# Kernel optimization log

Measured on AMD Instinct MI355X. Metric: run time of the kernel, lower is better.

## Reference

```python
import jax, jax.numpy as jnp
import numpy as np

B, C, H, W = 4, 256, 64, 64
CI = 3
TEMPERATURE = 0.0001 * 5
EPS = 2.220446049250313e-16  # sys.float_info.epsilon


def _nearest_up4(x):
    # nn.Upsample(scale_factor=4, mode='nearest'): [B,C,H,W] -> [B,C,4H,4W]
    return jnp.repeat(jnp.repeat(x, 4, axis=2), 4, axis=3)


def _avg_pool2(x):
    # AvgPool2d(kernel=2, stride=2, pad=0)
    b, c, h, w = x.shape
    return x.reshape(b, c, h // 2, 2, w // 2, 2).mean(axis=(3, 5))


def _center_norm(feats):
    # subtract per-channel spatial mean, then L2-normalize over channels per position
    b, c, h, w = feats.shape
    t = feats.reshape(b, c, h * w)
    t = t - t.mean(axis=-1, keepdims=True)
    n = jnp.linalg.norm(t, axis=1, keepdims=True) + EPS
    return t / n  # [B,C,HW]


def setup_inputs() -> dict:
    key = jax.random.key(0)
    k1, k2, k3 = jax.random.split(key, 3)
    return {
        "x_feats": jax.random.normal(k1, (B, C, H, W), jnp.float32),
        "y_feats": jax.random.normal(k2, (B, C, H, W), jnp.float32),
        "y_img": jax.random.uniform(k3, (B, CI, 4 * H, 4 * W), jnp.float32),
    }


def reference(x_feats, y_feats, y_img):
    b, c, h, w = x_feats.shape
    hw = h * w
    theta = _center_norm(x_feats)  # [B,C,HW]
    phi = _center_norm(y_feats)    # [B,C,HW]
    f = jnp.einsum('bcm,bcn->bmn', theta, phi)  # dense correlation [B,HW,HW]
    loss_feat_pair = jnp.mean(jnp.abs(theta - phi))  # F.l1_loss(theta, phi)
    # WTA_scale_weight == 1 -> WTA branch bypassed, just temperature scaling
    f_wta = f / TEMPERATURE
    f_div_c = jax.nn.softmax(f_wta, axis=-1)  # [B,HW,HW]
    # warped features: f_div_C @ y_feats^T
    b_lab = y_feats.reshape(b, c, hw)
    y = jnp.einsum('bmn,bcn->bcm', f_div_c, b_lab).reshape(b, c, h, w)
    # soft-argmax coordinates
    xc = (jnp.arange(hw) % w).astype(x_feats.dtype)   # [HW]
    yc = (jnp.arange(hw) // w).astype(x_feats.dtype)  # [HW]
    coords_x = f_div_c @ xc  # [B,HW]
    coords_y = f_div_c @ yc  # [B,HW]
    coords1 = jnp.stack([coords_x, coords_y], axis=1).reshape(b, 2, h, w)
    coords0 = jnp.stack([xc, yc], axis=0).reshape(1, 2, h, w)
    flow = _nearest_up4(coords1 - coords0)  # [B,2,4H,4W]
    # image warping branch (y_img is not None)
    yi = _avg_pool2(_avg_pool2(y_img))  # [B,CI,H,W]
    ci = yi.shape[1]
    yi_flat = yi.reshape(b, ci, hw)
    y_img_attn = jnp.einsum('bmn,bcn->bmc', f_div_c, yi_flat)  # [B,HW,CI]
    f_div_c_v = jax.nn.softmax(jnp.swapaxes(f_wta, 1, 2), axis=-1)
    y_img_cyc = jnp.einsum('bmn,bnc->bcm', f_div_c_v, y_img_attn).reshape(b, ci, h, w)
    y_img_out = jnp.swapaxes(y_img_attn, 1, 2).reshape(b, ci, h, w)
    return (y, flow, _nearest_up4(y_img_out), _nearest_up4(y_img_cyc), loss_feat_pair)
```

## Files before the change

kernel.cpp:

```cpp
#include <hip/hip_runtime.h>
#include <math.h>

#define HW   4096
#define NCH  256
#define NB   4

constexpr float TEMP  = (float)(0.0001 * 5.0);
constexpr float INV_T = 1.0f / TEMP;
constexpr float EPSN  = 2.220446049250313e-16f;

typedef __attribute__((ext_vector_type(8))) _Float16 f16x8;
typedef __attribute__((ext_vector_type(4))) float    f32x4;

constexpr size_t OFF_YT    = 0;
constexpr size_t OFF_YI    = OFF_YT    + (size_t)NB*HW*NCH;
constexpr size_t OFF_MEAN  = OFF_YI    + (size_t)NB*3*HW;
constexpr size_t OFF_RNORM = OFF_MEAN  + (size_t)2*NB*NCH;
constexpr size_t OFF_NSQP  = OFF_RNORM + (size_t)2*NB*HW;
constexpr size_t OFF_F     = OFF_NSQP  + (size_t)2*NB*8*HW;
constexpr size_t OFF_YP    = OFF_F     + (size_t)HW*HW;
constexpr size_t OFF_ROWP  = OFF_YP;
constexpr size_t OFF_COLP  = OFF_YP + (size_t)32*7*HW;
constexpr size_t OFF_RMAX  = OFF_YP    + (size_t)8*NCH*HW;
constexpr size_t OFF_RSUM  = OFF_RMAX  + HW;
constexpr size_t OFF_CMAX  = OFF_RSUM  + HW;
constexpr size_t OFF_CSUM  = OFF_CMAX  + HW;
constexpr size_t OFF_COORD = OFF_CSUM  + HW;
constexpr size_t OFF_ATTN  = OFF_COORD + (size_t)NB*2*HW;
constexpr size_t OFF_CYC   = OFF_ATTN  + (size_t)NB*HW*3;
constexpr size_t OFF_CYCP  = OFF_CYC   + (size_t)NB*3*HW;
constexpr size_t OFF_LOSSP = OFF_CYCP  + (size_t)32*3*HW;
constexpr size_t OFF_F16   = OFF_LOSSP + 1024;

constexpr size_t OUT_Y    = 0;
constexpr size_t OUT_FLOW = (size_t)NB*NCH*HW;
constexpr size_t OUT_IMG  = OUT_FLOW + (size_t)NB*2*256*256;
constexpr size_t OUT_CYCO = OUT_IMG  + (size_t)NB*3*256*256;
constexpr size_t OUT_LOSS = OUT_CYCO + (size_t)NB*3*256*256;

__device__ __forceinline__ void gload16(const void* g, void* l) {
    __builtin_amdgcn_global_load_lds(
        (const __attribute__((address_space(1))) unsigned int*)g,
        (__attribute__((address_space(3))) unsigned int*)l, 16, 0, 0);
}

__global__ void mean_kernel(const float* __restrict__ xf, const float* __restrict__ yf,
                            float* __restrict__ means) {
    const float* src = (blockIdx.y == 0 ? xf : yf) + (size_t)blockIdx.x * HW;
    float s = 0.f;
    for (int i = threadIdx.x; i < HW; i += 256) s += src[i];
    __shared__ float red[256];
    red[threadIdx.x] = s; __syncthreads();
    for (int st = 128; st > 0; st >>= 1) {
        if (threadIdx.x < st) red[threadIdx.x] += red[threadIdx.x + st];
        __syncthreads();
    }
    if (threadIdx.x == 0) means[blockIdx.y * (NB*NCH) + blockIdx.x] = red[0] * (1.0f / HW);
}

__global__ void nsq_partial_kernel(const float* __restrict__ xf, const float* __restrict__ yf,
                                   const float* __restrict__ means, float* __restrict__ part) {
    int t = blockIdx.z >> 2, b = blockIdx.z & 3;
    int m = blockIdx.x * 256 + threadIdx.x;
    int c0 = blockIdx.y * 32;
    const float* src = (t == 0 ? xf : yf) + (size_t)b * NCH * HW;
    const float* mn = means + t * (NB*NCH) + b * NCH;
    float acc = 0.f;
    for (int c = c0; c < c0 + 32; ++c) {
        float v = src[(size_t)c * HW + m] - mn[c];
        acc += v * v;
    }
    part[(((size_t)t*NB + b) * 8 + blockIdx.y) * HW + m] = acc;
}

__global__ void nsq_combine_kernel(const float* __restrict__ part, float* __restrict__ rnorms) {
    int t = blockIdx.y >> 2, b = blockIdx.y & 3;
    int m = blockIdx.x * 256 + threadIdx.x;
    const float* p = part + ((size_t)t*NB + b) * 8 * HW + m;
    float s = 0.f;
    for (int k = 0; k < 8; ++k) s += p[(size_t)k * HW];
    rnorms[((size_t)t*NB + b) * HW + m] = 1.0f / (sqrtf(s) + EPSN);
}

__global__ void ycast_kernel(const float* __restrict__ yf, _Float16* __restrict__ yf16) {
    size_t i = ((size_t)blockIdx.x * 256 + threadIdx.x) * 8;
    const float4* s = (const float4*)(yf + i);
    float4 v0 = s[0], v1 = s[1];
    f16x8 o;
    o[0]=(_Float16)v0.x; o[1]=(_Float16)v0.y; o[2]=(_Float16)v0.z; o[3]=(_Float16)v0.w;
    o[4]=(_Float16)v1.x; o[5]=(_Float16)v1.y; o[6]=(_Float16)v1.z; o[7]=(_Float16)v1.w;
    *(f16x8*)(yf16 + i) = o;
}

__global__ void prep_kernel(const float* __restrict__ xf, const float* __restrict__ yf,
                            const float* __restrict__ means,
                            _Float16* __restrict__ th, _Float16* __restrict__ tl,
                            _Float16* __restrict__ ph, _Float16* __restrict__ pl, int b) {
    __shared__ float tile[32][33];
    int t = blockIdx.z;
    int c0 = blockIdx.x * 32, m0 = blockIdx.y * 32;
    const float* src = (t == 0 ? xf : yf) + (size_t)b * NCH * HW;
    const float* mn  = means + t * (NB*NCH) + b * NCH;
    int tx = threadIdx.x & 31, ty = threadIdx.x >> 5;
    for (int i = ty; i < 32; i += 8)
        tile[i][tx] = src[(size_t)(c0 + i) * HW + m0 + tx] - mn[c0 + i];
    __syncthreads();
    _Float16* H = (t == 0 ? th : ph);
    _Float16* L = (t == 0 ? tl : pl);
    for (int i = ty; i < 32; i += 8) {
        float v = tile[tx][i];
        _Float16 h = (_Float16)v;
        _Float16 l = (_Float16)(v - (float)h);
        H[(size_t)(m0 + i)*NCH + c0 + tx] = h;
        L[(size_t)(m0 + i)*NCH + c0 + tx] = l;
    }
}

__global__ void avgpool_kernel(const float* __restrict__ yimg, float* __restrict__ yi) {
    size_t idx = (size_t)blockIdx.x * 256 + threadIdx.x;
    int m  = (int)(idx & (HW - 1));
    int bc = (int)(idx >> 12);
    int h = m >> 6, w = m & 63;
    const float* p = yimg + (size_t)bc * 65536 + (size_t)(h*4) * 256 + w*4;
    float s = 0.f;
    #pragma unroll
    for (int dy = 0; dy < 4; ++dy) {
        #pragma unroll
        for (int dx = 0; dx < 4; ++dx) s += p[dy*256 + dx];
    }
    yi[idx] = s * (1.0f/16.0f);
}

__global__ __launch_bounds__(256) void gemm_f_kernel(
        const _Float16* __restrict__ th, const _Float16* __restrict__ tl,
        const _Float16* __restrict__ ph, const _Float16* __restrict__ pl,
        const float* __restrict__ rnorms, const float* __restrict__ yi,
        float* __restrict__ f, float* __restrict__ rowp, float* __restrict__ colp,
        int b) {
    __shared__ char lds[2][4][8192];
    int tid  = threadIdx.x;
    int lane = tid & 63;
    int w = tid >> 6, wm = w >> 1, wn = w & 1;
    int m0 = blockIdx.y * 128, n0 = blockIdx.x * 128;

    int o0 = tid * 16, o1 = o0 + 4096;
    int r0 = o0 >> 6, s0 = (o0 >> 4) & 3, g0 = s0 ^ ((r0 >> 1) & 3);
    int r1 = o1 >> 6, s1 = (o1 >> 4) & 3, g1 = s1 ^ ((r1 >> 1) & 3);
    size_t ga0 = (size_t)(n0 + r0)*NCH + g0*8;
    size_t ga1 = (size_t)(n0 + r1)*NCH + g1*8;
    size_t gb0 = (size_t)(m0 + r0)*NCH + g0*8;
    size_t gb1 = (size_t)(m0 + r1)*NCH + g1*8;

    int fra = wm*64 + (lane & 15);
    int frb = wn*64 + (lane & 15);
    int ks  = lane >> 4;

    auto STAGE = [&](int buf, int k0) {
        gload16(ph + ga0 + k0, &lds[buf][0][o0]);
        gload16(ph + ga1 + k0, &lds[buf][0][o1]);
        gload16(pl + ga0 + k0, &lds[buf][1][o0]);
        gload16(pl + ga1 + k0, &lds[buf][1][o1]);
        gload16(th + gb0 + k0, &lds[buf][2][o0]);
        gload16(th + gb1 + k0, &lds[buf][2][o1]);
        gload16(tl + gb0 + k0, &lds[buf][3][o0]);
        gload16(tl + gb1 + k0, &lds[buf][3][o1]);
    };

    f32x4 acc[4][4];
    #pragma unroll
    for (int i = 0; i < 4; ++i)
        #pragma unroll
        for (int j = 0; j < 4; ++j) acc[i][j] = (f32x4){0.f, 0.f, 0.f, 0.f};

    STAGE(0, 0);
    __syncthreads();
    int cur = 0;
    for (int kt = 0; kt < 8; ++kt) {
        if (kt < 7) STAGE(cur ^ 1, (kt + 1) * 32);

        f16x8 ah[4], al[4], bh[4], bl[4];
        #pragma unroll
        for (int i = 0; i < 4; ++i) {
            int rowa = fra + i*16;
            int offa = rowa*64 + ((ks ^ ((rowa >> 1) & 3)) << 4);
            ah[i] = *(const f16x8*)&lds[cur][0][offa];
            al[i] = *(const f16x8*)&lds[cur][1][offa];
            int rowb = frb + i*16;
            int offb = rowb*64 + ((ks ^ ((rowb >> 1) & 3)) << 4);
            bh[i] = *(const f16x8*)&lds[cur][2][offb];
            bl[i] = *(const f16x8*)&lds[cur][3][offb];
        }
        #pragma unroll
        for (int i = 0; i < 4; ++i)
            #pragma unroll
            for (int j = 0; j < 4; ++j) {
                acc[i][j] = __builtin_amdgcn_mfma_f32_16x16x32_f16(ah[i], bh[j], acc[i][j], 0, 0, 0);
                acc[i][j] = __builtin_amdgcn_mfma_f32_16x16x32_f16(ah[i], bl[j], acc[i][j], 0, 0, 0);
                acc[i][j] = __builtin_amdgcn_mfma_f32_16x16x32_f16(al[i], bh[j], acc[i][j], 0, 0, 0);
            }
        __syncthreads();
        cur ^= 1;
    }

    const float* rnx = rnorms + (size_t)b * HW;
    const float* rny = rnorms + (size_t)(NB + b) * HW;
    int mg[4];  float rxv[4];
    #pragma unroll
    for (int j = 0; j < 4; ++j) {
        mg[j] = m0 + wn*64 + j*16 + (lane & 15);
        rxv[j] = rnx[mg[j]];
    }
    int nl0 = wm*64 + (lane >> 4)*4;
    #pragma unroll
    for (int i = 0; i < 4; ++i)
        #pragma unroll
        for (int r = 0; r < 4; ++r) {
            float ry = rny[n0 + nl0 + i*16 + r];
            #pragma unroll
            for (int j = 0; j < 4; ++j) acc[i][j][r] *= rxv[j] * ry;
        }

    #pragma unroll
    for (int j = 0; j < 4; ++j)
        #pragma unroll
        for (int i = 0; i < 4; ++i)
            *(f32x4*)&f[(size_t)mg[j]*HW + n0 + nl0 + i*16] = acc[i][j];

    float* S     = (float*)&lds[0][0][0];
    float* rowm  = S;
    float* sums6 = S + 256;
    float* colm  = S + 1792;
    float* colsm = S + 2048;

    #pragma unroll
    for (int j = 0; j < 4; ++j) {
        float v = acc[0][j][0];
        #pragma unroll
        for (int i = 0; i < 4; ++i)
            #pragma unroll
            for (int r = 0; r < 4; ++r) v = fmaxf(v, acc[i][j][r]);
        v = fmaxf(v, __shfl_xor(v, 16));
        v = fmaxf(v, __shfl_xor(v, 32));
        if ((lane >> 4) == 0) rowm[wm*128 + wn*64 + j*16 + lane] = v;
    }
    #pragma unroll
    for (int i = 0; i < 4; ++i)
        #pragma unroll
        for (int r = 0; r < 4; ++r) {
            float v = fmaxf(fmaxf(acc[i][0][r], acc[i][1][r]),
                            fmaxf(acc[i][2][r], acc[i][3][r]));
            #pragma unroll
            for (int d = 1; d < 16; d <<= 1) v = fmaxf(v, __shfl_xor(v, d));
            if ((lane & 15) == 0) colm[wn*128 + wm*64 + i*16 + (lane >> 4)*4 + r] = v;
        }
    __syncthreads();

    float bm[4];
    #pragma unroll
    for (int j = 0; j < 4; ++j) {
        int ml = wn*64 + j*16 + (lane & 15);
        bm[j] = fmaxf(rowm[ml], rowm[128 + ml]);
    }
    float a6[4][6];
    #pragma unroll
    for (int j = 0; j < 4; ++j)
        #pragma unroll
        for (int q = 0; q < 6; ++q) a6[j][q] = 0.f;
    const float* yib = yi + (size_t)b * 3 * HW;
    #pragma unroll
    for (int i = 0; i < 4; ++i)
        #pragma unroll
        for (int r = 0; r < 4; ++r) {
            int ng = n0 + nl0 + i*16 + r;
            float xc = (float)(ng & 63), yc = (float)(ng >> 6);
            float y0 = yib[ng], y1 = yib[HW + ng], y2 = yib[2*HW + ng];
            #pragma unroll
            for (int j = 0; j < 4; ++j) {
                float e = __expf((acc[i][j][r] - bm[j]) * INV_T);
                a6[j][0] += e;      a6[j][1] += e*xc; a6[j][2] += e*yc;
                a6[j][3] += e*y0;   a6[j][4] += e*y1; a6[j][5] += e*y2;
            }
        }
    #pragma unroll
    for (int j = 0; j < 4; ++j)
        #pragma unroll
        for (int q = 0; q < 6; ++q) {
            float v = a6[j][q];
            v += __shfl_xor(v, 16);
            v += __shfl_xor(v, 32);
            if ((lane >> 4) == 0) sums6[(wm*128 + wn*64 + j*16 + lane)*6 + q] = v;
        }
    #pragma unroll
    for (int i = 0; i < 4; ++i)
        #pragma unroll
        for (int r = 0; r < 4; ++r) {
            int nl = wm*64 + i*16 + (lane >> 4)*4 + r;
            float cm = fmaxf(colm[nl], colm[128 + nl]);
            float cs = 0.f;
            #pragma unroll
            for (int j = 0; j < 4; ++j) cs += __expf((acc[i][j][r] - cm) * INV_T);
            #pragma unroll
            for (int d = 1; d < 16; d <<= 1) cs += __shfl_xor(cs, d);
            if ((lane & 15) == 0) colsm[wn*128 + nl] = cs;
        }
    __syncthreads();

    if (tid < 128) {
        int ml = tid;
        float m2 = fmaxf(rowm[ml], rowm[128 + ml]);
        rowp[((size_t)blockIdx.x*7 + 0)*HW + m0 + ml] = m2;
        #pragma unroll
        for (int q = 0; q < 6; ++q)
            rowp[((size_t)blockIdx.x*7 + 1 + q)*HW + m0 + ml] =
                sums6[ml*6 + q] + sums6[(128 + ml)*6 + q];
    } else {
        int nl = tid - 128;
        float c2 = fmaxf(colm[nl], colm[128 + nl]);
        colp[((size_t)blockIdx.y*2 + 0)*HW + n0 + nl] = c2;
        colp[((size_t)blockIdx.y*2 + 1)*HW + n0 + nl] = colsm[nl] + colsm[128 + nl];
    }
}

__global__ void rowcol_combine_kernel(const float* __restrict__ rowp,
        const float* __restrict__ colp,
        float* __restrict__ rmax, float* __restrict__ rsuminv,
        float* __restrict__ coords, float* __restrict__ attn,
        float* __restrict__ cmax, float* __restrict__ csuminv, int b) {
    int idx = blockIdx.x * 256 + threadIdx.x;
    if (blockIdx.y == 0) {
        int m = idx;
        float gm = -3.0e38f;
        for (int t = 0; t < 32; ++t) gm = fmaxf(gm, rowp[((size_t)t*7)*HW + m]);
        float S=0, CX=0, CY=0, A0=0, A1=0, A2=0;
        for (int t = 0; t < 32; ++t) {
            const float* p = rowp + (size_t)t*7*HW + m;
            float wgt = __expf((p[0] - gm) * INV_T);
            S  += p[1*HW] * wgt; CX += p[2*HW] * wgt; CY += p[3*HW] * wgt;
            A0 += p[4*HW] * wgt; A1 += p[5*HW] * wgt; A2 += p[6*HW] * wgt;
        }
        float inv = 1.0f / S;
        rmax[m] = gm; rsuminv[m] = inv;
        coords[((size_t)b*2 + 0)*HW + m] = CX * inv;
        coords[((size_t)b*2 + 1)*HW + m] = CY * inv;
        attn[((size_t)b*HW + m)*3 + 0] = A0 * inv;
        attn[((size_t)b*HW + m)*3 + 1] = A1 * inv;
        attn[((size_t)b*HW + m)*3 + 2] = A2 * inv;
    } else {
        int n = idx;
        float gm = -3.0e38f;
        for (int t = 0; t < 32; ++t) gm = fmaxf(gm, colp[((size_t)t*2)*HW + n]);
        float S = 0.f;
        for (int t = 0; t < 32; ++t) {
            const float* p = colp + (size_t)t*2*HW + n;
            S += p[1*HW] * __expf((p[0] - gm) * INV_T);
        }
        cmax[n] = gm;
        csuminv[n] = 1.0f / S;
    }
}

__global__ __launch_bounds__(512) void gemm_y_kernel(const float* __restrict__ f,
        const float* __restrict__ rmax, const _Float16* __restrict__ yf16,
        float* __restrict__ yp, int b) {
    __shared__ __align__(16) char ldsA[4096];
    __shared__ __align__(16) char ldsB[16384];
    int tid  = threadIdx.x;
    int lane = tid & 63;
    int w = tid >> 6, wm = w >> 2, wn = w & 3;
    int m0 = blockIdx.x * 64;
    int ks = blockIdx.y;
    const _Float16* Yb = yf16 + (size_t)b * NCH * HW;

    int ar = (tid & 255) >> 2, akc = tid & 3;
    int aoff = ar*64 + ((akc ^ ((ar >> 1) & 3)) << 4);
    float arm = rmax[m0 + ar];
    const float* frow = f + (size_t)(m0 + ar)*HW + akc*8;

    int o0 = tid*16, o1 = o0 + 8192;
    int br0 = o0 >> 6, bs0 = (o0 >> 4) & 3, bg0 = bs0 ^ ((br0 >> 1) & 3);
    int br1 = o1 >> 6, bs1 = (o1 >> 4) & 3, bg1 = bs1 ^ ((br1 >> 1) & 3);
    size_t gb0 = (size_t)br0*HW + bg0*8;
    size_t gb1 = (size_t)br1*HW + bg1*8;

    int fra = wm*32 + (lane & 15);
    int frb = wn*64 + (lane & 15);
    int kslot = lane >> 4;

    f32x4 acc[2][4];
    #pragma unroll
    for (int i = 0; i < 2; ++i)
        #pragma unroll
        for (int j = 0; j < 4; ++j) acc[i][j] = (f32x4){0.f, 0.f, 0.f, 0.f};

    for (int k0 = ks*1024; k0 < ks*1024 + 1024; k0 += 32) {
        gload16(Yb + gb0 + k0, &ldsB[o0]);
        gload16(Yb + gb1 + k0, &ldsB[o1]);
        if (tid < 256) {
            const float4* fp = (const float4*)(frow + k0);
            float4 v0 = fp[0], v1 = fp[1];
            f16x8 pk;
            pk[0] = (_Float16)__expf((v0.x - arm) * INV_T);
            pk[1] = (_Float16)__expf((v0.y - arm) * INV_T);
            pk[2] = (_Float16)__expf((v0.z - arm) * INV_T);
            pk[3] = (_Float16)__expf((v0.w - arm) * INV_T);
            pk[4] = (_Float16)__expf((v1.x - arm) * INV_T);
            pk[5] = (_Float16)__expf((v1.y - arm) * INV_T);
            pk[6] = (_Float16)__expf((v1.z - arm) * INV_T);
            pk[7] = (_Float16)__expf((v1.w - arm) * INV_T);
            *(f16x8*)&ldsA[aoff] = pk;
        }
        __syncthreads();

        f16x8 af[2], bf[4];
        #pragma unroll
        for (int i = 0; i < 2; ++i) {
            int rowa = fra + i*16;
            af[i] = *(const f16x8*)&ldsA[rowa*64 + ((kslot ^ ((rowa >> 1) & 3)) << 4)];
        }
        #pragma unroll
        for (int j = 0; j < 4; ++j) {
            int rowb = frb + j*16;
            bf[j] = *(const f16x8*)&ldsB[rowb*64 + ((kslot ^ ((rowb >> 1) & 3)) << 4)];
        }
        #pragma unroll
        for (int i = 0; i < 2; ++i)
            #pragma unroll
            for (int j = 0; j < 4; ++j)
                acc[i][j] = __builtin_amdgcn_mfma_f32_16x16x32_f16(af[i], bf[j], acc[i][j], 0, 0, 0);
        __syncthreads();
    }

    #pragma unroll
    for (int i = 0; i < 2; ++i) {
        int m = m0 + wm*32 + i*16 + (lane >> 4) * 4;
        #pragma unroll
        for (int j = 0; j < 4; ++j) {
            int c = wn*64 + j*16 + (lane & 15);
            *(f32x4*)(yp + ((size_t)ks*NCH + c)*HW + m) = acc[i][j];
        }
    }
}

__global__ void ycombine_kernel(const float* __restrict__ yp, const float* __restrict__ rsuminv,
                                float* __restrict__ out, int b) {
    size_t idx = (size_t)blockIdx.x * 256 + threadIdx.x;
    int m = (int)(idx & (HW - 1));
    float s = 0.f;
    #pragma unroll
    for (int k = 0; k < 4; ++k) s += yp[(size_t)k*NCH*HW + idx];
    out[OUT_Y + (size_t)b*NCH*HW + idx] = s * rsuminv[m];
}

__global__ __launch_bounds__(256) void cyc_partial_kernel(const float* __restrict__ f,
        const float* __restrict__ cmax, const float* __restrict__ attn,
        float* __restrict__ part, int b) {
    __shared__ float at[128*3];
    int i  = blockIdx.x * 256 + threadIdx.x;
    int j0 = blockIdx.y * 128;
    for (int k = threadIdx.x; k < 384; k += 256)
        at[k] = attn[((size_t)b*HW + j0)*3 + k];
    __syncthreads();
    float cm = cmax[i];
    float a0=0, a1=0, a2=0;
    for (int jj = 0; jj < 128; ++jj) {
        float e = __expf((f[(size_t)(j0+jj)*HW + i] - cm) * INV_T);
        a0 = fmaf(e, at[jj*3+0], a0);
        a1 = fmaf(e, at[jj*3+1], a1);
        a2 = fmaf(e, at[jj*3+2], a2);
    }
    part[((size_t)blockIdx.y*3 + 0)*HW + i] = a0;
    part[((size_t)blockIdx.y*3 + 1)*HW + i] = a1;
    part[((size_t)blockIdx.y*3 + 2)*HW + i] = a2;
}

__global__ void cyc_combine_kernel(const float* __restrict__ part, const float* __restrict__ csuminv,
                                   float* __restrict__ cyc, int b) {
    int i = blockIdx.x * 256 + threadIdx.x;
    int c = blockIdx.y;
    float s = 0.f;
    for (int k = 0; k < 32; ++k) s += part[((size_t)k*3 + c)*HW + i];
    cyc[((size_t)b*3 + c)*HW + i] = s * csuminv[i];
}

__global__ void flow_kernel(const float* __restrict__ coords, float* __restrict__ out) {
    size_t idx = (size_t)blockIdx.x * 256 + threadIdx.x;
    int x4 = (int)(idx & 255);
    int y4 = (int)((idx >> 8) & 255);
    int ch = (int)((idx >> 16) & 1);
    int b  = (int)(idx >> 17);
    int w = x4 >> 2, h = y4 >> 2;
    int m = h*64 + w;
    float c1 = coords[((size_t)b*2 + ch)*HW + m];
    float c0 = (ch == 0) ? (float)w : (float)h;
    out[OUT_FLOW + idx] = c1 - c0;
}

__global__ void imgout_kernel(const float* __restrict__ attn, const float* __restrict__ cyc,
                              float* __restrict__ out) {
    size_t idx = (size_t)blockIdx.x * 256 + threadIdx.x;
    int x4 = (int)(idx & 255);
    int y4 = (int)((idx >> 8) & 255);
    int rest = (int)(idx >> 16);
    int ch = rest % 3, b = rest / 3;
    int m = (y4 >> 2)*64 + (x4 >> 2);
    out[OUT_IMG  + idx] = attn[((size_t)b*HW + m)*3 + ch];
    out[OUT_CYCO + idx] = cyc[((size_t)b*3 + ch)*HW + m];
}

__global__ void loss_partial_kernel(const float* __restrict__ xf, const float* __restrict__ yf,
                                    const float* __restrict__ means, const float* __restrict__ rnorms,
                                    float* __restrict__ part) {
    __shared__ float red[256];
    size_t base = (size_t)blockIdx.x * 4096;
    float s = 0.f;
    for (int k = 0; k < 16; ++k) {
        size_t id = base + (size_t)k*256 + threadIdx.x;
        int m  = (int)(id & (HW - 1));
        int bc = (int)(id >> 12);
        int b  = bc >> 8;
        float th = (xf[id] - means[bc])          * rnorms[(size_t)b*HW + m];
        float ph = (yf[id] - means[NB*NCH + bc]) * rnorms[(size_t)(NB + b)*HW + m];
        s += fabsf(th - ph);
    }
    red[threadIdx.x] = s; __syncthreads();
    for (int st = 128; st > 0; st >>= 1) {
        if (threadIdx.x < st) red[threadIdx.x] += red[threadIdx.x + st];
        __syncthreads();
    }
    if (threadIdx.x == 0) part[blockIdx.x] = red[0];
}

__global__ void loss_final_kernel(const float* __restrict__ part, float* __restrict__ out) {
    __shared__ float red[256];
    float s = 0.f;
    for (int k = threadIdx.x; k < 1024; k += 256) s += part[k];
    red[threadIdx.x] = s; __syncthreads();
    for (int st = 128; st > 0; st >>= 1) {
        if (threadIdx.x < st) red[threadIdx.x] += red[threadIdx.x + st];
        __syncthreads();
    }
    if (threadIdx.x == 0) out[OUT_LOSS] = red[0] * (1.0f / 4194304.0f);
}

extern "C" void kernel_launch(void* const* d_in, const int* in_sizes, int n_in,
                              void* d_out, int out_size, void* d_ws, size_t ws_size,
                              hipStream_t stream) {
    (void)in_sizes; (void)n_in; (void)out_size; (void)ws_size;
    const float* xf   = (const float*)d_in[0];
    const float* yf   = (const float*)d_in[1];
    const float* yimg = (const float*)d_in[2];
    float* out = (float*)d_out;
    float* ws  = (float*)d_ws;

    _Float16* yf16 = (_Float16*)(ws + OFF_YT);
    float* yi      = ws + OFF_YI;
    float* means   = ws + OFF_MEAN;
    float* rnorms  = ws + OFF_RNORM;
    float* nsqp    = ws + OFF_NSQP;
    float* fbuf    = ws + OFF_F;
    float* yp      = ws + OFF_YP;
    float* rowp    = ws + OFF_ROWP;
    float* colp    = ws + OFF_COLP;
    float* rmax    = ws + OFF_RMAX;
    float* rsuminv = ws + OFF_RSUM;
    float* cmax    = ws + OFF_CMAX;
    float* csuminv = ws + OFF_CSUM;
    float* coords  = ws + OFF_COORD;
    float* attn    = ws + OFF_ATTN;
    float* cyc     = ws + OFF_CYC;
    float* cycp    = ws + OFF_CYCP;
    float* lossp   = ws + OFF_LOSSP;
    _Float16* th = (_Float16*)(ws + OFF_F16);
    _Float16* tl = th + (size_t)HW*NCH;
    _Float16* ph = tl + (size_t)HW*NCH;
    _Float16* pl = ph + (size_t)HW*NCH;

    mean_kernel        <<<dim3(NB*NCH, 2),   256, 0, stream>>>(xf, yf, means);
    nsq_partial_kernel <<<dim3(16, 8, 8),    256, 0, stream>>>(xf, yf, means, nsqp);
    nsq_combine_kernel <<<dim3(16, 8),       256, 0, stream>>>(nsqp, rnorms);
    ycast_kernel       <<<2048,              256, 0, stream>>>(yf, yf16);
    avgpool_kernel     <<<NB*3*HW/256,       256, 0, stream>>>(yimg, yi);

    for (int b = 0; b < NB; ++b) {
        prep_kernel          <<<dim3(8, 128, 2), 256, 0, stream>>>(xf, yf, means, th, tl, ph, pl, b);
        gemm_f_kernel        <<<dim3(32, 32),    256, 0, stream>>>(th, tl, ph, pl, rnorms, yi,
                                                                   fbuf, rowp, colp, b);
        rowcol_combine_kernel<<<dim3(16, 2),     256, 0, stream>>>(rowp, colp, rmax, rsuminv,
                                                                   coords, attn, cmax, csuminv, b);
        gemm_y_kernel        <<<dim3(64, 4),     512, 0, stream>>>(fbuf, rmax, yf16, yp, b);
        ycombine_kernel      <<<NCH*HW/256,      256, 0, stream>>>(yp, rsuminv, out, b);
        cyc_partial_kernel   <<<dim3(16, 32),    256, 0, stream>>>(fbuf, cmax, attn, cycp, b);
        cyc_combine_kernel   <<<dim3(16, 3),     256, 0, stream>>>(cycp, csuminv, cyc, b);
    }

    flow_kernel        <<<NB*2*65536/256, 256, 0, stream>>>(coords, out);
    imgout_kernel      <<<NB*3*65536/256, 256, 0, stream>>>(attn, cyc, out);
    loss_partial_kernel<<<1024,           256, 0, stream>>>(xf, yf, means, rnorms, lossp);
    loss_final_kernel  <<<1,              256, 0, stream>>>(lossp, out);
}
```

Before: 534.3 us.

## Store block-local fp16 softmax numerators instead of fp32 logits, rescale downstream

The correlation GEMM now computes the row- and column-softmax exponentials against block-local maxima and stores them as two fp16 matrices, plus per-block maxima, instead of writing the full fp32 logit matrix. The value GEMM and the cycle kernel read these fp16 values and apply a cheap per-block correction factor, so they no longer recompute exponentials over the whole HWxHW matrix. The partial Y results are also stored in fp16. This halves bytes per element but writes two matrices, and it adds precision risk: fp16 exponentials relative to a block maximum can underflow, and the final sums are now done on fp16 partials.

```diff
diff --git a/kernel.cpp b/kernel.cpp
--- a/kernel.cpp
+++ b/kernel.cpp
@@ -10,6 +10,7 @@
 constexpr float EPSN  = 2.220446049250313e-16f;
 
 typedef __attribute__((ext_vector_type(8))) _Float16 f16x8;
+typedef __attribute__((ext_vector_type(4))) _Float16 f16x4;
 typedef __attribute__((ext_vector_type(4))) float    f32x4;
 
 constexpr size_t OFF_YT    = 0;
@@ -17,15 +18,17 @@
 constexpr size_t OFF_MEAN  = OFF_YI    + (size_t)NB*3*HW;
 constexpr size_t OFF_RNORM = OFF_MEAN  + (size_t)2*NB*NCH;
 constexpr size_t OFF_NSQP  = OFF_RNORM + (size_t)2*NB*HW;
-constexpr size_t OFF_F     = OFF_NSQP  + (size_t)2*NB*8*HW;
-constexpr size_t OFF_YP    = OFF_F     + (size_t)HW*HW;
+constexpr size_t OFF_PB    = OFF_NSQP  + (size_t)2*NB*8*HW;
+constexpr size_t OFF_YP    = OFF_PB    + (size_t)HW*HW;
 constexpr size_t OFF_ROWP  = OFF_YP;
 constexpr size_t OFF_COLP  = OFF_YP + (size_t)32*7*HW;
 constexpr size_t OFF_RMAX  = OFF_YP    + (size_t)8*NCH*HW;
 constexpr size_t OFF_RSUM  = OFF_RMAX  + HW;
 constexpr size_t OFF_CMAX  = OFF_RSUM  + HW;
 constexpr size_t OFF_CSUM  = OFF_CMAX  + HW;
-constexpr size_t OFF_COORD = OFF_CSUM  + HW;
+constexpr size_t OFF_RMB   = OFF_CSUM  + HW;
+constexpr size_t OFF_CMB   = OFF_RMB   + (size_t)32*HW;
+constexpr size_t OFF_COORD = OFF_CMB   + (size_t)32*HW;
 constexpr size_t OFF_ATTN  = OFF_COORD + (size_t)NB*2*HW;
 constexpr size_t OFF_CYC   = OFF_ATTN  + (size_t)NB*HW*3;
 constexpr size_t OFF_CYCP  = OFF_CYC   + (size_t)NB*3*HW;
@@ -135,8 +138,9 @@
         const _Float16* __restrict__ th, const _Float16* __restrict__ tl,
         const _Float16* __restrict__ ph, const _Float16* __restrict__ pl,
         const float* __restrict__ rnorms, const float* __restrict__ yi,
-        float* __restrict__ f, float* __restrict__ rowp, float* __restrict__ colp,
-        int b) {
+        _Float16* __restrict__ Pbr, _Float16* __restrict__ Pbc,
+        float* __restrict__ rowp, float* __restrict__ colp,
+        float* __restrict__ rmb, float* __restrict__ cmb, int b) {
     __shared__ char lds[2][4][8192];
     int tid  = threadIdx.x;
     int lane = tid & 63;
@@ -220,12 +224,6 @@
             for (int j = 0; j < 4; ++j) acc[i][j][r] *= rxv[j] * ry;
         }
 
-    #pragma unroll
-    for (int j = 0; j < 4; ++j)
-        #pragma unroll
-        for (int i = 0; i < 4; ++i)
-            *(f32x4*)&f[(size_t)mg[j]*HW + n0 + nl0 + i*16] = acc[i][j];
-
     float* S     = (float*)&lds[0][0][0];
     float* rowm  = S;
     float* sums6 = S + 256;
@@ -268,19 +266,41 @@
         for (int q = 0; q < 6; ++q) a6[j][q] = 0.f;
     const float* yib = yi + (size_t)b * 3 * HW;
     #pragma unroll
-    for (int i = 0; i < 4; ++i)
+    for (int i = 0; i < 4; ++i) {
+        float er[4][4], ec[4][4];
         #pragma unroll
         for (int r = 0; r < 4; ++r) {
-            int ng = n0 + nl0 + i*16 + r;
+            int nl = nl0 + i*16 + r;
+            int ng = n0 + nl;
             float xc = (float)(ng & 63), yc = (float)(ng >> 6);
             float y0 = yib[ng], y1 = yib[HW + ng], y2 = yib[2*HW + ng];
+            float cm = fmaxf(colm[nl], colm[128 + nl]);
+            float cs = 0.f;
             #pragma unroll
             for (int j = 0; j < 4; ++j) {
-                float e = __expf((acc[i][j][r] - bm[j]) * INV_T);
+                float av = acc[i][j][r];
+                float e = __expf((av - bm[j]) * INV_T);
+                er[r][j] = e;
                 a6[j][0] += e;      a6[j][1] += e*xc; a6[j][2] += e*yc;
                 a6[j][3] += e*y0;   a6[j][4] += e*y1; a6[j][5] += e*y2;
+                float ev = __expf((av - cm) * INV_T);
+                ec[r][j] = ev;
+                cs += ev;
             }
-        }
+            #pragma unroll
+            for (int d = 1; d < 16; d <<= 1) cs += __shfl_xor(cs, d);
+            if ((lane & 15) == 0) colsm[wn*128 + nl] = cs;
+        }
+        #pragma unroll
+        for (int j = 0; j < 4; ++j) {
+            f16x4 pr, pc;
+            #pragma unroll
+            for (int r = 0; r < 4; ++r) { pr[r] = (_Float16)er[r][j]; pc[r] = (_Float16)ec[r][j]; }
+            size_t base = (size_t)mg[j]*HW + n0 + nl0 + i*16;
+            *(f16x4*)(Pbr + base) = pr;
+            *(f16x4*)(Pbc + base) = pc;
+        }
+    }
     #pragma unroll
     for (int j = 0; j < 4; ++j)
         #pragma unroll
@@ -290,25 +310,13 @@
             v += __shfl_xor(v, 32);
             if ((lane >> 4) == 0) sums6[(wm*128 + wn*64 + j*16 + lane)*6 + q] = v;
         }
-    #pragma unroll
-    for (int i = 0; i < 4; ++i)
-        #pragma unroll
-        for (int r = 0; r < 4; ++r) {
-            int nl = wm*64 + i*16 + (lane >> 4)*4 + r;
-            float cm = fmaxf(colm[nl], colm[128 + nl]);
-            float cs = 0.f;
-            #pragma unroll
-            for (int j = 0; j < 4; ++j) cs += __expf((acc[i][j][r] - cm) * INV_T);
-            #pragma unroll
-            for (int d = 1; d < 16; d <<= 1) cs += __shfl_xor(cs, d);
-            if ((lane & 15) == 0) colsm[wn*128 + nl] = cs;
-        }
     __syncthreads();
 
     if (tid < 128) {
         int ml = tid;
         float m2 = fmaxf(rowm[ml], rowm[128 + ml]);
         rowp[((size_t)blockIdx.x*7 + 0)*HW + m0 + ml] = m2;
+        rmb[(size_t)blockIdx.x*HW + m0 + ml] = m2;
         #pragma unroll
         for (int q = 0; q < 6; ++q)
             rowp[((size_t)blockIdx.x*7 + 1 + q)*HW + m0 + ml] =
@@ -317,6 +325,7 @@
         int nl = tid - 128;
         float c2 = fmaxf(colm[nl], colm[128 + nl]);
         colp[((size_t)blockIdx.y*2 + 0)*HW + n0 + nl] = c2;
+        cmb[(size_t)blockIdx.y*HW + n0 + nl] = c2;
         colp[((size_t)blockIdx.y*2 + 1)*HW + n0 + nl] = colsm[nl] + colsm[128 + nl];
     }
 }
@@ -359,9 +368,9 @@
     }
 }
 
-__global__ __launch_bounds__(512) void gemm_y_kernel(const float* __restrict__ f,
-        const float* __restrict__ rmax, const _Float16* __restrict__ yf16,
-        float* __restrict__ yp, int b) {
+__global__ __launch_bounds__(512) void gemm_y_kernel(const _Float16* __restrict__ Pbr,
+        const float* __restrict__ rmax, const float* __restrict__ rmb,
+        const _Float16* __restrict__ yf16, _Float16* __restrict__ yph, int b) {
     __shared__ __align__(16) char ldsA[4096];
     __shared__ __align__(16) char ldsB[16384];
     int tid  = threadIdx.x;
@@ -373,8 +382,9 @@
 
     int ar = (tid & 255) >> 2, akc = tid & 3;
     int aoff = ar*64 + ((akc ^ ((ar >> 1) & 3)) << 4);
-    float arm = rmax[m0 + ar];
-    const float* frow = f + (size_t)(m0 + ar)*HW + akc*8;
+    float gm = rmax[m0 + ar];
+    const _Float16* prow = Pbr + (size_t)(m0 + ar)*HW + akc*8;
+    const float* rmbm = rmb + (m0 + ar);
 
     int o0 = tid*16, o1 = o0 + 8192;
     int br0 = o0 >> 6, bs0 = (o0 >> 4) & 3, bg0 = bs0 ^ ((br0 >> 1) & 3);
@@ -392,21 +402,17 @@
         #pragma unroll
         for (int j = 0; j < 4; ++j) acc[i][j] = (f32x4){0.f, 0.f, 0.f, 0.f};
 
+    _Float16 corrh = (_Float16)0.f;
     for (int k0 = ks*1024; k0 < ks*1024 + 1024; k0 += 32) {
         gload16(Yb + gb0 + k0, &ldsB[o0]);
         gload16(Yb + gb1 + k0, &ldsB[o1]);
         if (tid < 256) {
-            const float4* fp = (const float4*)(frow + k0);
-            float4 v0 = fp[0], v1 = fp[1];
+            if ((k0 & 127) == 0)
+                corrh = (_Float16)__expf((rmbm[(size_t)(k0 >> 7)*HW] - gm) * INV_T);
+            f16x8 pb = *(const f16x8*)(prow + k0);
             f16x8 pk;
-            pk[0] = (_Float16)__expf((v0.x - arm) * INV_T);
-            pk[1] = (_Float16)__expf((v0.y - arm) * INV_T);
-            pk[2] = (_Float16)__expf((v0.z - arm) * INV_T);
-            pk[3] = (_Float16)__expf((v0.w - arm) * INV_T);
-            pk[4] = (_Float16)__expf((v1.x - arm) * INV_T);
-            pk[5] = (_Float16)__expf((v1.y - arm) * INV_T);
-            pk[6] = (_Float16)__expf((v1.z - arm) * INV_T);
-            pk[7] = (_Float16)__expf((v1.w - arm) * INV_T);
+            #pragma unroll
+            for (int q = 0; q < 8; ++q) pk[q] = pb[q] * corrh;
             *(f16x8*)&ldsA[aoff] = pk;
         }
         __syncthreads();
@@ -436,34 +442,38 @@
         #pragma unroll
         for (int j = 0; j < 4; ++j) {
             int c = wn*64 + j*16 + (lane & 15);
-            *(f32x4*)(yp + ((size_t)ks*NCH + c)*HW + m) = acc[i][j];
-        }
-    }
-}
-
-__global__ void ycombine_kernel(const float* __restrict__ yp, const float* __restrict__ rsuminv,
+            f16x4 v;
+            #pragma unroll
+            for (int r = 0; r < 4; ++r) v[r] = (_Float16)acc[i][j][r];
+            *(f16x4*)(yph + ((size_t)ks*NCH + c)*HW + m) = v;
+        }
+    }
+}
+
+__global__ void ycombine_kernel(const _Float16* __restrict__ yph, const float* __restrict__ rsuminv,
                                 float* __restrict__ out, int b) {
     size_t idx = (size_t)blockIdx.x * 256 + threadIdx.x;
     int m = (int)(idx & (HW - 1));
     float s = 0.f;
     #pragma unroll
-    for (int k = 0; k < 4; ++k) s += yp[(size_t)k*NCH*HW + idx];
+    for (int k = 0; k < 4; ++k) s += (float)yph[(size_t)k*NCH*HW + idx];
     out[OUT_Y + (size_t)b*NCH*HW + idx] = s * rsuminv[m];
 }
 
-__global__ __launch_bounds__(256) void cyc_partial_kernel(const float* __restrict__ f,
-        const float* __restrict__ cmax, const float* __restrict__ attn,
-        float* __restrict__ part, int b) {
+__global__ __launch_bounds__(256) void cyc_partial_kernel(const _Float16* __restrict__ Pbc,
+        const float* __restrict__ cmax, const float* __restrict__ cmb,
+        const float* __restrict__ attn, float* __restrict__ part, int b) {
     __shared__ float at[128*3];
     int i  = blockIdx.x * 256 + threadIdx.x;
     int j0 = blockIdx.y * 128;
+    int tm = blockIdx.y;
     for (int k = threadIdx.x; k < 384; k += 256)
         at[k] = attn[((size_t)b*HW + j0)*3 + k];
     __syncthreads();
-    float cm = cmax[i];
+    float corrc = __expf((cmb[(size_t)tm*HW + i] - cmax[i]) * INV_T);
     float a0=0, a1=0, a2=0;
     for (int jj = 0; jj < 128; ++jj) {
-        float e = __expf((f[(size_t)(j0+jj)*HW + i] - cm) * INV_T);
+        float e = (float)Pbc[(size_t)(j0+jj)*HW + i] * corrc;
         a0 = fmaf(e, at[jj*3+0], a0);
         a1 = fmaf(e, at[jj*3+1], a1);
         a2 = fmaf(e, at[jj*3+2], a2);
@@ -557,14 +567,17 @@
     float* means   = ws + OFF_MEAN;
     float* rnorms  = ws + OFF_RNORM;
     float* nsqp    = ws + OFF_NSQP;
-    float* fbuf    = ws + OFF_F;
-    float* yp      = ws + OFF_YP;
+    _Float16* Pbr  = (_Float16*)(ws + OFF_PB);
+    _Float16* Pbc  = Pbr + (size_t)HW*HW;
+    _Float16* yph  = (_Float16*)(ws + OFF_YP);
     float* rowp    = ws + OFF_ROWP;
     float* colp    = ws + OFF_COLP;
     float* rmax    = ws + OFF_RMAX;
     float* rsuminv = ws + OFF_RSUM;
     float* cmax    = ws + OFF_CMAX;
     float* csuminv = ws + OFF_CSUM;
+    float* rmb     = ws + OFF_RMB;
+    float* cmb     = ws + OFF_CMB;
     float* coords  = ws + OFF_COORD;
     float* attn    = ws + OFF_ATTN;
     float* cyc     = ws + OFF_CYC;
@@ -584,13 +597,13 @@
     for (int b = 0; b < NB; ++b) {
         prep_kernel          <<<dim3(8, 128, 2), 256, 0, stream>>>(xf, yf, means, th, tl, ph, pl, b);
         gemm_f_kernel        <<<dim3(32, 32),    256, 0, stream>>>(th, tl, ph, pl, rnorms, yi,
-                                                                   fbuf, rowp, colp, b);
+                                                                   Pbr, Pbc, rowp, colp, rmb, cmb, b);
         rowcol_combine_kernel<<<dim3(16, 2),     256, 0, stream>>>(rowp, colp, rmax, rsuminv,
                                                                    coords, attn, cmax, csuminv, b);
-        gemm_y_kernel        <<<dim3(64, 4),     512, 0, stream>>>(fbuf, rmax, yf16, yp, b);
-        ycombine_kernel      <<<NCH*HW/256,      256, 0, stream>>>(yp, rsuminv, out, b);
-        cyc_partial_kernel   <<<dim3(16, 32),    256, 0, stream>>>(fbuf, cmax, attn, cycp, b);
+        cyc_partial_kernel   <<<dim3(16, 32),    256, 0, stream>>>(Pbc, cmax, cmb, attn, cycp, b);
         cyc_combine_kernel   <<<dim3(16, 3),     256, 0, stream>>>(cycp, csuminv, cyc, b);
+        gemm_y_kernel        <<<dim3(64, 4),     512, 0, stream>>>(Pbr, rmax, rmb, yf16, yph, b);
+        ycombine_kernel      <<<NCH*HW/256,      256, 0, stream>>>(yph, rsuminv, out, b);
     }
 
     flow_kernel        <<<NB*2*65536/256, 256, 0, stream>>>(coords, out);
```

After: 591.6 us. 1.11x slower.
